# Performance work log

Hardware: AMD Instinct MI355X
Metric: run time of the kernel (lower is better)

Reference implementation:

```python
import jax, jax.numpy as jnp
import numpy as np

K = 32        # neighbors kept
SCALE = 1     # dilation stride for dilated kNN


def setup_inputs() -> dict:
    key = jax.random.key(0)
    ks = jax.random.split(key, 8)
    s = 0.05  # weight init scale
    return {
        "x": jax.random.normal(ks[0], (16, 3, 4096), jnp.float32),
        "w1": jax.random.normal(ks[1], (64, 3), jnp.float32) * s,
        "b1": jnp.zeros((64,), jnp.float32),
        "w2": jax.random.normal(ks[2], (128, 64), jnp.float32) * s,
        "b2": jnp.zeros((128,), jnp.float32),
        "w3": jax.random.normal(ks[3], (1024, 128), jnp.float32) * s,
        "b3": jnp.zeros((1024,), jnp.float32),
        "fw1": jax.random.normal(ks[4], (512, 1024), jnp.float32) * s,
        "fb1": jnp.zeros((512,), jnp.float32),
        "fw2": jax.random.normal(ks[5], (256, 512), jnp.float32) * s,
        "fb2": jnp.zeros((256,), jnp.float32),
        "fw3": jax.random.normal(ks[6], (9, 256), jnp.float32) * s,
        "fb3": jnp.zeros((9,), jnp.float32),
    }


def _knn_idx(x):
    # x: (B, C, N). Returns (B, N, K) indices of K nearest neighbors (dilated by SCALE).
    inner = jnp.einsum('bcn,bcm->bnm', x, x)            # (B, N, N)
    sq = jnp.sum(x * x, axis=1)                          # (B, N)
    neg_dist = 2.0 * inner - sq[:, :, None] - sq[:, None, :]  # = -||xi-xj||^2
    _, idx = jax.lax.top_k(neg_dist, K * SCALE)          # (B, N, K*SCALE)
    return idx[:, :, ::SCALE]                            # (B, N, K)


def reference(x, w1, b1, w2, b2, w3, b3, fw1, fb1, fw2, fb2, fw3, fb3):
    B, C, N = x.shape
    idx = _knn_idx(x)                                    # (B, N, K)
    xt = jnp.swapaxes(x, 1, 2)                           # (B, N, C)
    # gather neighbors: nbrs[b,n,k,c] = xt[b, idx[b,n,k], c]
    nbrs = jax.vmap(lambda xb, ib: xb[ib])(xt, idx)      # (B, N, K, C)
    x0 = nbrs - xt[:, :, None, :]                        # edge features x_j - x_i

    # STN (T-Net): shared MLP over edges, global max pool, FC head -> 3x3 transform
    h = jax.nn.relu(jnp.einsum('bnkc,oc->bnko', x0, w1) + b1)
    h = jax.nn.relu(jnp.einsum('bnkc,oc->bnko', h, w2) + b2)
    h = jax.nn.relu(jnp.einsum('bnkc,oc->bnko', h, w3) + b3)
    g = jnp.max(h, axis=(1, 2))                          # (B, 1024)
    f = jax.nn.relu(g @ fw1.T + fb1)
    f = jax.nn.relu(f @ fw2.T + fb2)
    t = (f @ fw3.T + fb3).reshape(B, 3, 3) + jnp.eye(3, dtype=x.dtype)

    out = jnp.einsum('bnc,bcd->bnd', xt, t)              # bmm(x^T, t)
    return jnp.swapaxes(out, 1, 2)                       # (B, 3, N)
```

## Files before the change

### kernel.cpp

```cpp
#include <hip/hip_runtime.h>
#include <hip/hip_fp8.h>

typedef __bf16 bf16_t;
typedef __bf16 bf16x8 __attribute__((ext_vector_type(8)));
typedef float floatx16 __attribute__((ext_vector_type(16)));
typedef int intx8 __attribute__((ext_vector_type(8)));
typedef unsigned long long u64;

#define B_ 16
#define N_ 4096
#define K_ 32


__device__ __forceinline__ unsigned enc_f(float f) {
    unsigned u = __float_as_uint(f);
    return (u & 0x80000000u) ? ~u : (u | 0x80000000u);
}
__device__ __forceinline__ float dec_f(unsigned e) {
    return __uint_as_float((e & 0x80000000u) ? (e & 0x7fffffffu) : ~e);
}

__device__ __forceinline__ float max3f(float a, float b, float c) {
    float d;
    asm("v_max3_f32 %0, %1, %2, %3" : "=v"(d) : "v"(a), "v"(b), "v"(c));
    return d;
}

__device__ __forceinline__ void ce(unsigned& a, unsigned& b) {
    const unsigned mn = a < b ? a : b;
    const unsigned mx = a < b ? b : a;
    a = mn; b = mx;
}

__global__ __launch_bounds__(512, 4) void knn_kernel(
    const float* __restrict__ x, const float* __restrict__ w3,
    const float* __restrict__ w2, unsigned short* __restrict__ idxb,
    unsigned* __restrict__ g_enc, unsigned char* __restrict__ w3f8,
    bf16_t* __restrict__ w2sw)
{
    __shared__ __align__(16) float4 cand[16 * 257];
    unsigned* lists = (unsigned*)cand;
    unsigned* m1 = ((unsigned*)cand) + 8192;
    const int tid = threadIdx.x;
    const int bid = blockIdx.x;

    {
        const int g = bid * 512 + tid;
        if (g < 131072) {
            const int j  = g & 31;
            const int lI = (g >> 5) & 63;
            const int kq = (g >> 11) & 1;
            const int cb = g >> 12;
            const int mt2 = kq * 2 + (j >> 4), q = j & 15;
            const int lmI = lI & 31, hiI = lI >> 5;
            const int ch = mt2 * 32 + (q & 3) + 8 * (q >> 2) + 4 * hiI;
            __hip_fp8_e4m3 t(16.0f * w3[(cb * 32 + lmI) * 128 + ch]);
            w3f8[g] = t.__x;
        } else if (g < 139264) {
            const int o = g - 131072;
            const int f = o >> 9, r = o & 511, lI = r >> 3, jj = r & 7;
            const int ks = f & 3, nb = f >> 2, lmI = lI & 31, hiI = lI >> 5;
            const int ic = ks * 16 + 4 * hiI + 8 * (jj >> 2) + (jj & 3);
            w2sw[o] = (bf16_t)w2[(nb * 32 + lmI) * 64 + ic];
        } else if (g < 155648) {
            g_enc[g - 139264] = 0u;
        }
    }

    const int b  = bid >> 7;
    const int q  = tid >> 4;
    const int n  = (bid & 127) * 32 + q;
    const int t  = tid & 15;
    const float* xb = x + b * 3 * N_;

    for (int j = tid; j < N_; j += 512) {
        float cx = xb[j], cy = xb[N_ + j], cz = xb[2 * N_ + j];
        cand[j + (j >> 8)] = make_float4(-2.f * cx, -2.f * cy, -2.f * cz,
                                         fmaf(cx, cx, fmaf(cy, cy, cz * cz)));
    }
    __syncthreads();

    const float xi0 = xb[n], xi1 = xb[N_ + n], xi2 = xb[2 * N_ + n];
    const float xisq1 = fmaf(xi0, xi0, fmaf(xi1, xi1, xi2 * xi2)) + 1.0f;

    unsigned r[8];
    #pragma unroll
    for (int s = 0; s < 8; s++) r[s] = 0x7F7FFFFFu;

    const int j0 = t * 256;
    const int pb = t * 257;
    #pragma unroll 1
    for (int jb = 0; jb < 256; jb += 8) {
        unsigned k[8];
        #pragma unroll
        for (int u = 0; u < 8; u++) {
            const float4 c = cand[pb + jb + u];
            const float d = fmaf(c.z, xi2, fmaf(c.y, xi1, fmaf(c.x, xi0, c.w)));
            k[u] = (__float_as_uint(d + xisq1) & 0xFFFFF000u)
                 | (unsigned)(j0 + jb + u);
        }
        ce(k[0], k[1]); ce(k[2], k[3]); ce(k[4], k[5]); ce(k[6], k[7]);
        ce(k[0], k[2]); ce(k[1], k[3]); ce(k[4], k[6]); ce(k[5], k[7]);
        ce(k[1], k[2]); ce(k[5], k[6]);
        ce(k[0], k[4]); ce(k[1], k[5]); ce(k[2], k[6]); ce(k[3], k[7]);
        ce(k[2], k[4]); ce(k[3], k[5]);
        ce(k[1], k[2]); ce(k[3], k[4]); ce(k[5], k[6]);
        unsigned s[8];
        #pragma unroll
        for (int u = 0; u < 8; u++)
            s[u] = r[u] < k[7 - u] ? r[u] : k[7 - u];
        ce(s[0], s[4]); ce(s[1], s[5]); ce(s[2], s[6]); ce(s[3], s[7]);
        ce(s[0], s[2]); ce(s[1], s[3]); ce(s[4], s[6]); ce(s[5], s[7]);
        ce(s[0], s[1]); ce(s[2], s[3]); ce(s[4], s[5]); ce(s[6], s[7]);
        #pragma unroll
        for (int u = 0; u < 8; u++) r[u] = s[u];
    }
    __syncthreads();

    #pragma unroll
    for (int k = 0; k < 8; k++) lists[tid * 9 + k] = r[k];
    __syncthreads();

    if (tid < 128) {
        const int q1 = tid >> 2, gi = tid & 3;
        const int base = (q1 * 16 + gi * 4) * 9;
        unsigned h0 = lists[base], h1 = lists[base + 9];
        unsigned h2 = lists[base + 18], h3 = lists[base + 27];
        int p0 = 0, p1 = 0, p2 = 0, p3 = 0;
        unsigned* outp = m1 + (q1 * 4 + gi) * 32;
        #pragma unroll 1
        for (int k = 0; k < 32; k++) {
            const unsigned m01 = h0 < h1 ? h0 : h1;
            const unsigned m23 = h2 < h3 ? h2 : h3;
            const unsigned v = m01 < m23 ? m01 : m23;
            outp[k] = v;
            if (m01 < m23) {
                if (h1 < h0) { p1++; h1 = p1 < 8 ? lists[base + 9 + p1] : 0xFFFFFFFFu; }
                else         { p0++; h0 = p0 < 8 ? lists[base + p0]     : 0xFFFFFFFFu; }
            } else {
                if (h3 < h2) { p3++; h3 = p3 < 8 ? lists[base + 27 + p3] : 0xFFFFFFFFu; }
                else         { p2++; h2 = p2 < 8 ? lists[base + 18 + p2] : 0xFFFFFFFFu; }
            }
        }
    }
    __syncthreads();

    if (tid < 32) {
        const unsigned* g0 = m1 + tid * 128;
        unsigned h0 = g0[0], h1 = g0[32], h2 = g0[64], h3 = g0[96];
        int p0 = 0, p1 = 0, p2 = 0, p3 = 0;
        const int nq = (bid & 127) * 32 + tid;
        unsigned short* op = idxb + ((size_t)(b * N_ + nq)) * K_;
        #pragma unroll 1
        for (int k = 0; k < K_; k++) {
            const unsigned m01 = h0 < h1 ? h0 : h1;
            const unsigned m23 = h2 < h3 ? h2 : h3;
            const unsigned v = m01 < m23 ? m01 : m23;
            op[k] = (unsigned short)(v & 0xFFFu);
            if (m01 < m23) {
                if (h1 < h0) { p1++; h1 = p1 < 32 ? g0[32 + p1] : 0xFFFFFFFFu; }
                else         { p0++; h0 = p0 < 32 ? g0[p0]      : 0xFFFFFFFFu; }
            } else {
                if (h3 < h2) { p3++; h3 = p3 < 32 ? g0[96 + p3] : 0xFFFFFFFFu; }
                else         { p2++; h2 = p2 < 32 ? g0[64 + p2] : 0xFFFFFFFFu; }
            }
        }
    }
}

__device__ __forceinline__ void chunk_epilogue(
    const floatx16& a0, const floatx16& a1, int cb, unsigned* gl, int lm)
{
    float c0 = fmaxf(a0[0], a1[0]);
    float c1 = fmaxf(a0[1], a1[1]);
    float c2 = fmaxf(a0[2], a1[2]);
    float c3 = fmaxf(a0[3], a1[3]);
    #pragma unroll
    for (int o = 4; o < 16; o += 4) {
        c0 = max3f(a0[o + 0], a1[o + 0], c0);
        c1 = max3f(a0[o + 1], a1[o + 1], c1);
        c2 = max3f(a0[o + 2], a1[o + 2], c2);
        c3 = max3f(a0[o + 3], a1[o + 3], c3);
    }
    const float m = max3f(c0, c1, fmaxf(c2, c3));
    atomicMax(&gl[cb * 32 + lm], enc_f(m));
}

__global__ __launch_bounds__(256, 3) void mlp_kernel(
    const float* __restrict__ x, const unsigned short* __restrict__ idxb,
    const float* __restrict__ w1, const float* __restrict__ b1,
    const float* __restrict__ b2,
    const bf16_t* __restrict__ w2sw, const unsigned char* __restrict__ w3f8,
    unsigned* __restrict__ g_enc)
{
    __shared__ unsigned gl[1024];
    __shared__ __align__(16) float4 w1l[64];
    __shared__ __align__(16) float b2s[128];

    const int tid = threadIdx.x;
    const int b   = blockIdx.x >> 9;
    const int p0  = (blockIdx.x & 511) * 8;
    const float* xb = x + b * 3 * N_;

    const int wv = tid >> 6;
    const int l  = tid & 63;
    const int lm = l & 31;
    const int hi = l >> 5;

    for (int i = tid; i < 1024; i += 256) gl[i] = 0u;
    if (tid < 64)
        w1l[tid] = make_float4(w1[tid * 3], w1[tid * 3 + 1], w1[tid * 3 + 2], b1[tid]);
    else if (tid < 192)
        b2s[tid - 64] = 256.0f * b2[tid - 64];
    __syncthreads();

    const floatx16 zf = (floatx16)0.f;

    const unsigned char* w3p = w3f8 + l * 32;
#define PREFETCH_W3(dst, c) do {                                              \
        dst[0] = *(const intx8*)(w3p + (c) * 4096);                           \
        dst[1] = *(const intx8*)(w3p + (c) * 4096 + 2048);                    \
    } while (0)

    intx8 bwA[2], bwB[2];
    PREFETCH_W3(bwA, 0);

    float d0[2], d1[2], d2[2];
    #pragma unroll
    for (int nt2 = 0; nt2 < 2; nt2++) {
        const int pp = p0 + wv * 2 + nt2;
        const int j  = idxb[((size_t)(b * N_ + pp)) * K_ + lm];
        d0[nt2] = xb[j]          - xb[pp];
        d1[nt2] = xb[N_ + j]     - xb[N_ + pp];
        d2[nt2] = xb[2 * N_ + j] - xb[2 * N_ + pp];
    }

    bf16x8 a1f[2];
    #pragma unroll
    for (int tt = 0; tt < 2; tt++) {
        const float4 w = w1l[tt * 32 + lm];
        bf16x8 v = (bf16x8)(bf16_t)0.f;
        if (hi == 0) {
            v[0] = (bf16_t)w.x; v[1] = (bf16_t)w.y;
            v[2] = (bf16_t)w.z; v[3] = (bf16_t)w.w;
        }
        a1f[tt] = v;
    }

    bf16x8 b1h[2][4];
    #pragma unroll
    for (int nt2 = 0; nt2 < 2; nt2++) {
        bf16x8 bf = (bf16x8)(bf16_t)0.f;
        if (hi == 0) {
            bf[0] = (bf16_t)d0[nt2]; bf[1] = (bf16_t)d1[nt2];
            bf[2] = (bf16_t)d2[nt2]; bf[3] = (bf16_t)1.0f;
        }
        floatx16 hacc[2];
        hacc[0] = __builtin_amdgcn_mfma_f32_32x32x16_bf16(a1f[0], bf, zf, 0, 0, 0);
        hacc[1] = __builtin_amdgcn_mfma_f32_32x32x16_bf16(a1f[1], bf, zf, 0, 0, 0);
        #pragma unroll
        for (int ks = 0; ks < 4; ks++)
            #pragma unroll
            for (int jj = 0; jj < 8; jj++)
                b1h[nt2][ks][jj] = (bf16_t)fmaxf(
                    hacc[ks >> 1][(jj & 3) + 4 * (jj >> 2) + 8 * (ks & 1)], 0.f);
    }

    intx8 a3v[2][2];
    #pragma unroll
    for (int mt2 = 0; mt2 < 4; mt2++) {
        floatx16 acc0 = (floatx16)0.f, acc1 = (floatx16)0.f;
        #pragma unroll
        for (int ks = 0; ks < 4; ks++) {
            const bf16x8 aw = *(const bf16x8*)&w2sw[((mt2 * 4 + ks) * 64 + l) * 8];
            acc0 = __builtin_amdgcn_mfma_f32_32x32x16_bf16(aw, b1h[0][ks], acc0, 0, 0, 0);
            acc1 = __builtin_amdgcn_mfma_f32_32x32x16_bf16(aw, b1h[1][ks], acc1, 0, 0, 0);
        }
        const int kq = mt2 >> 1, c0 = (mt2 & 1) * 4;
        #pragma unroll
        for (int i2 = 0; i2 < 4; i2++) {
            const float4 bb = *(const float4*)&b2s[mt2 * 32 + i2 * 8 + hi * 4];
            {
                const float v0 = fmaxf(fmaf(acc0[4 * i2 + 0], 256.f, bb.x), 0.f);
                const float v1 = fmaxf(fmaf(acc0[4 * i2 + 1], 256.f, bb.y), 0.f);
                const float v2 = fmaxf(fmaf(acc0[4 * i2 + 2], 256.f, bb.z), 0.f);
                const float v3 = fmaxf(fmaf(acc0[4 * i2 + 3], 256.f, bb.w), 0.f);
                int w = __builtin_amdgcn_cvt_pk_fp8_f32(v0, v1, 0, false);
                w = __builtin_amdgcn_cvt_pk_fp8_f32(v2, v3, w, true);
                a3v[0][kq][c0 + i2] = w;
            }
            {
                const float v0 = fmaxf(fmaf(acc1[4 * i2 + 0], 256.f, bb.x), 0.f);
                const float v1 = fmaxf(fmaf(acc1[4 * i2 + 1], 256.f, bb.y), 0.f);
                const float v2 = fmaxf(fmaf(acc1[4 * i2 + 2], 256.f, bb.z), 0.f);
                const float v3 = fmaxf(fmaf(acc1[4 * i2 + 3], 256.f, bb.w), 0.f);
                int w = __builtin_amdgcn_cvt_pk_fp8_f32(v0, v1, 0, false);
                w = __builtin_amdgcn_cvt_pk_fp8_f32(v2, v3, w, true);
                a3v[1][kq][c0 + i2] = w;
            }
        }
    }

#define COMPUTE_W3(d0_, d1_, buf) do {                                        \
        __builtin_amdgcn_s_setprio(1);                                        \
        d0_ = __builtin_amdgcn_mfma_scale_f32_32x32x64_f8f6f4(                \
            a3v[0][0], buf[0], zf, 0, 0, 0, 0x7F7F7F7F, 0, 0x7F7F7F7F);       \
        d1_ = __builtin_amdgcn_mfma_scale_f32_32x32x64_f8f6f4(                \
            a3v[1][0], buf[0], zf, 0, 0, 0, 0x7F7F7F7F, 0, 0x7F7F7F7F);       \
        d0_ = __builtin_amdgcn_mfma_scale_f32_32x32x64_f8f6f4(                \
            a3v[0][1], buf[1], d0_, 0, 0, 0, 0x7F7F7F7F, 0, 0x7F7F7F7F);      \
        d1_ = __builtin_amdgcn_mfma_scale_f32_32x32x64_f8f6f4(                \
            a3v[1][1], buf[1], d1_, 0, 0, 0, 0x7F7F7F7F, 0, 0x7F7F7F7F);      \
        __builtin_amdgcn_s_setprio(0); } while (0)

    floatx16 pA0, pA1, pB0, pB1;

    PREFETCH_W3(bwB, 1);
    COMPUTE_W3(pA0, pA1, bwA);

    #pragma unroll 1
    for (int cc = 0; cc < 15; cc++) {
        PREFETCH_W3(bwA, 2 * cc + 2);
        COMPUTE_W3(pB0, pB1, bwB);
        chunk_epilogue(pA0, pA1, 2 * cc, gl, lm);
        PREFETCH_W3(bwB, 2 * cc + 3);
        COMPUTE_W3(pA0, pA1, bwA);
        chunk_epilogue(pB0, pB1, 2 * cc + 1, gl, lm);
    }
    COMPUTE_W3(pB0, pB1, bwB);
    chunk_epilogue(pA0, pA1, 30, gl, lm);
    chunk_epilogue(pB0, pB1, 31, gl, lm);

#undef PREFETCH_W3
#undef COMPUTE_W3

    __syncthreads();
    for (int i = tid; i < 1024; i += 256)
        atomicMax(&g_enc[b * 1024 + i], gl[i]);
}

__global__ __launch_bounds__(256) void head1_kernel(
    const unsigned* __restrict__ g_enc, const float* __restrict__ b3,
    const float* __restrict__ fw1, const float* __restrict__ fb1,
    float* __restrict__ f1buf)
{
    __shared__ __align__(16) float g[1024];
    __shared__ float red[256];
    const int t = threadIdx.x;
    const int b = blockIdx.x >> 3;
    const int s = blockIdx.x & 7;

    for (int i = t; i < 1024; i += 256)
        g[i] = fmaxf(fmaf(dec_f(g_enc[b * 1024 + i]), 2.44140625e-4f, b3[i]), 0.f);
    __syncthreads();

    const int o = s * 64 + (t & 63);
    const int quarter = t >> 6;
    const float4* wr = (const float4*)(fw1 + (size_t)o * 1024) + quarter * 64;
    const float4* gv = (const float4*)g + quarter * 64;
    float acc = 0.f;
    #pragma unroll 4
    for (int i = 0; i < 64; i++) {
        float4 a = wr[i], c = gv[i];
        acc = fmaf(a.x, c.x, acc); acc = fmaf(a.y, c.y, acc);
        acc = fmaf(a.z, c.z, acc); acc = fmaf(a.w, c.w, acc);
    }
    red[t] = acc;
    __syncthreads();
    if (t < 64) {
        const float v = red[t] + red[t + 64] + red[t + 128] + red[t + 192];
        f1buf[b * 512 + s * 64 + t] = fmaxf(v + fb1[s * 64 + t], 0.f);
    }
}

__global__ __launch_bounds__(256) void head2_kernel(
    const float* __restrict__ f1buf,
    const float* __restrict__ fw2, const float* __restrict__ fb2,
    const float* __restrict__ fw3, const float* __restrict__ fb3,
    float* __restrict__ tmat)
{
    __shared__ __align__(16) float f1[512];
    __shared__ __align__(16) float f2[256];
    const int t = threadIdx.x, b = blockIdx.x;

    if (t < 128) ((float4*)f1)[t] = ((const float4*)(f1buf + b * 512))[t];
    __syncthreads();
    {
        const int o = t;
        const float4* wr = (const float4*)(fw2 + (size_t)o * 512);
        const float4* fv = (const float4*)f1;
        float acc = fb2[o];
        for (int i = 0; i < 128; i++) {
            float4 a = wr[i], c = fv[i];
            acc = fmaf(a.x, c.x, acc); acc = fmaf(a.y, c.y, acc);
            acc = fmaf(a.z, c.z, acc); acc = fmaf(a.w, c.w, acc);
        }
        f2[o] = fmaxf(acc, 0.f);
    }
    __syncthreads();
    if (t < 9) {
        const float4* wr = (const float4*)(fw3 + (size_t)t * 256);
        const float4* fv = (const float4*)f2;
        float acc = fb3[t];
        for (int i = 0; i < 64; i++) {
            float4 a = wr[i], c = fv[i];
            acc = fmaf(a.x, c.x, acc); acc = fmaf(a.y, c.y, acc);
            acc = fmaf(a.z, c.z, acc); acc = fmaf(a.w, c.w, acc);
        }
        if (t == 0 || t == 4 || t == 8) acc += 1.f;
        tmat[b * 9 + t] = acc;
    }
}

__global__ __launch_bounds__(256) void out_kernel(
    const float* __restrict__ x, const float* __restrict__ tmat,
    float* __restrict__ out)
{
    const int gid = blockIdx.x * 256 + threadIdx.x;
    const int b = gid >> 12, n = gid & 4095;
    const float* T = tmat + b * 9;
    const float x0 = x[b * 12288 + n];
    const float x1 = x[b * 12288 + 4096 + n];
    const float x2 = x[b * 12288 + 8192 + n];
    #pragma unroll
    for (int d = 0; d < 3; d++)
        out[b * 12288 + d * 4096 + n] =
            fmaf(x2, T[6 + d], fmaf(x1, T[3 + d], x0 * T[d]));
}

extern "C" void kernel_launch(void* const* d_in, const int* in_sizes, int n_in,
                              void* d_out, int out_size, void* d_ws, size_t ws_size,
                              hipStream_t stream) {
    const float* x   = (const float*)d_in[0];
    const float* w1  = (const float*)d_in[1];
    const float* b1  = (const float*)d_in[2];
    const float* w2  = (const float*)d_in[3];
    const float* b2  = (const float*)d_in[4];
    const float* w3  = (const float*)d_in[5];
    const float* b3  = (const float*)d_in[6];
    const float* fw1 = (const float*)d_in[7];
    const float* fb1 = (const float*)d_in[8];
    const float* fw2 = (const float*)d_in[9];
    const float* fb2 = (const float*)d_in[10];
    const float* fw3 = (const float*)d_in[11];
    const float* fb3 = (const float*)d_in[12];
    float* out = (float*)d_out;

    char* ws = (char*)d_ws;
    unsigned short* idxb = (unsigned short*)ws;
    unsigned* g_enc = (unsigned*)(ws + 4194304);
    unsigned char* w3f8 = (unsigned char*)(ws + 4259840);
    bf16_t* w2sw = (bf16_t*)(ws + 4390912);
    float* tmat  = (float*)(ws + 4407296);
    float* f1buf = (float*)(ws + 4407872);

    knn_kernel<<<2048, 512, 0, stream>>>(x, w3, w2, idxb, g_enc, w3f8, w2sw);
    mlp_kernel<<<8192, 256, 0, stream>>>(x, idxb, w1, b1, b2, w2sw, w3f8, g_enc);
    head1_kernel<<<128, 256, 0, stream>>>(g_enc, b3, fw1, fb1, f1buf);
    head2_kernel<<<16, 256, 0, stream>>>(f1buf, fw2, fb2, fw3, fb3, tmat);
    out_kernel<<<256, 256, 0, stream>>>(x, tmat, out);
}
```

Measured before the change: 465.4 us.

## Process two queries per thread in kNN scan and reorder W3 prefetch pipeline

```diff
diff --git a/kernel.cpp b/kernel.cpp
--- a/kernel.cpp
+++ b/kernel.cpp
@@ -30,6 +30,26 @@
     const unsigned mn = a < b ? a : b;
     const unsigned mx = a < b ? b : a;
     a = mn; b = mx;
+}
+
+__device__ __forceinline__ void sort8(unsigned* k) {
+    ce(k[0], k[1]); ce(k[2], k[3]); ce(k[4], k[5]); ce(k[6], k[7]);
+    ce(k[0], k[2]); ce(k[1], k[3]); ce(k[4], k[6]); ce(k[5], k[7]);
+    ce(k[1], k[2]); ce(k[5], k[6]);
+    ce(k[0], k[4]); ce(k[1], k[5]); ce(k[2], k[6]); ce(k[3], k[7]);
+    ce(k[2], k[4]); ce(k[3], k[5]);
+    ce(k[1], k[2]); ce(k[3], k[4]); ce(k[5], k[6]);
+}
+__device__ __forceinline__ void merge_top8(unsigned* r, const unsigned* k) {
+    unsigned s[8];
+    #pragma unroll
+    for (int u = 0; u < 8; u++)
+        s[u] = r[u] < k[7 - u] ? r[u] : k[7 - u];
+    ce(s[0], s[4]); ce(s[1], s[5]); ce(s[2], s[6]); ce(s[3], s[7]);
+    ce(s[0], s[2]); ce(s[1], s[3]); ce(s[4], s[6]); ce(s[5], s[7]);
+    ce(s[0], s[1]); ce(s[2], s[3]); ce(s[4], s[5]); ce(s[6], s[7]);
+    #pragma unroll
+    for (int u = 0; u < 8; u++) r[u] = s[u];
 }
 
 __global__ __launch_bounds__(512, 4) void knn_kernel(
@@ -68,9 +88,8 @@
     }
 
     const int b  = bid >> 7;
-    const int q  = tid >> 4;
-    const int n  = (bid & 127) * 32 + q;
-    const int t  = tid & 15;
+    const int qp = tid >> 5;
+    const int ch = tid & 31;
     const float* xb = x + b * 3 * N_;
 
     for (int j = tid; j < N_; j += 512) {
@@ -80,54 +99,49 @@
     }
     __syncthreads();
 
-    const float xi0 = xb[n], xi1 = xb[N_ + n], xi2 = xb[2 * N_ + n];
-    const float xisq1 = fmaf(xi0, xi0, fmaf(xi1, xi1, xi2 * xi2)) + 1.0f;
-
-    unsigned r[8];
-    #pragma unroll
-    for (int s = 0; s < 8; s++) r[s] = 0x7F7FFFFFu;
-
-    const int j0 = t * 256;
-    const int pb = t * 257;
+    const int na = (bid & 127) * 32 + qp;
+    const int nb = na + 16;
+    const float qa0 = xb[na], qa1 = xb[N_ + na], qa2 = xb[2 * N_ + na];
+    const float qb0 = xb[nb], qb1 = xb[N_ + nb], qb2 = xb[2 * N_ + nb];
+    const float sqa = fmaf(qa0, qa0, fmaf(qa1, qa1, qa2 * qa2)) + 1.0f;
+    const float sqb = fmaf(qb0, qb0, fmaf(qb1, qb1, qb2 * qb2)) + 1.0f;
+
+    unsigned ra[8], rb[8];
+    #pragma unroll
+    for (int s = 0; s < 8; s++) { ra[s] = 0x7F7FFFFFu; rb[s] = 0x7F7FFFFFu; }
+
+    const int j0 = ch * 128;
+    const int pb = ch * 128 + (ch >> 1);
     #pragma unroll 1
-    for (int jb = 0; jb < 256; jb += 8) {
-        unsigned k[8];
+    for (int jb = 0; jb < 128; jb += 8) {
+        unsigned ka[8], kb[8];
         #pragma unroll
         for (int u = 0; u < 8; u++) {
             const float4 c = cand[pb + jb + u];
-            const float d = fmaf(c.z, xi2, fmaf(c.y, xi1, fmaf(c.x, xi0, c.w)));
-            k[u] = (__float_as_uint(d + xisq1) & 0xFFFFF000u)
-                 | (unsigned)(j0 + jb + u);
-        }
-        ce(k[0], k[1]); ce(k[2], k[3]); ce(k[4], k[5]); ce(k[6], k[7]);
-        ce(k[0], k[2]); ce(k[1], k[3]); ce(k[4], k[6]); ce(k[5], k[7]);
-        ce(k[1], k[2]); ce(k[5], k[6]);
-        ce(k[0], k[4]); ce(k[1], k[5]); ce(k[2], k[6]); ce(k[3], k[7]);
-        ce(k[2], k[4]); ce(k[3], k[5]);
-        ce(k[1], k[2]); ce(k[3], k[4]); ce(k[5], k[6]);
-        unsigned s[8];
-        #pragma unroll
-        for (int u = 0; u < 8; u++)
-            s[u] = r[u] < k[7 - u] ? r[u] : k[7 - u];
-        ce(s[0], s[4]); ce(s[1], s[5]); ce(s[2], s[6]); ce(s[3], s[7]);
-        ce(s[0], s[2]); ce(s[1], s[3]); ce(s[4], s[6]); ce(s[5], s[7]);
-        ce(s[0], s[1]); ce(s[2], s[3]); ce(s[4], s[5]); ce(s[6], s[7]);
-        #pragma unroll
-        for (int u = 0; u < 8; u++) r[u] = s[u];
-    }
-    __syncthreads();
-
-    #pragma unroll
-    for (int k = 0; k < 8; k++) lists[tid * 9 + k] = r[k];
-    __syncthreads();
-
-    if (tid < 128) {
-        const int q1 = tid >> 2, gi = tid & 3;
-        const int base = (q1 * 16 + gi * 4) * 9;
-        unsigned h0 = lists[base], h1 = lists[base + 9];
-        unsigned h2 = lists[base + 18], h3 = lists[base + 27];
+            const float da = fmaf(c.z, qa2, fmaf(c.y, qa1, fmaf(c.x, qa0, c.w)));
+            const float db = fmaf(c.z, qb2, fmaf(c.y, qb1, fmaf(c.x, qb0, c.w)));
+            ka[u] = (__float_as_uint(da + sqa) & 0xFFFFF000u) | (unsigned)(j0 + jb + u);
+            kb[u] = (__float_as_uint(db + sqb) & 0xFFFFF000u) | (unsigned)(j0 + jb + u);
+        }
+        sort8(ka); merge_top8(ra, ka);
+        sort8(kb); merge_top8(rb, kb);
+    }
+    __syncthreads();
+
+    #pragma unroll
+    for (int k = 0; k < 8; k++) {
+        lists[((qp * 32 + ch) << 3) + k]        = ra[k];
+        lists[(((qp + 16) * 32 + ch) << 3) + k] = rb[k];
+    }
+    __syncthreads();
+
+    if (tid < 256) {
+        const int q1 = tid >> 3, gi = tid & 7;
+        const int base = (q1 * 32 + gi * 4) * 8;
+        unsigned h0 = lists[base], h1 = lists[base + 8];
+        unsigned h2 = lists[base + 16], h3 = lists[base + 24];
         int p0 = 0, p1 = 0, p2 = 0, p3 = 0;
-        unsigned* outp = m1 + (q1 * 4 + gi) * 32;
+        unsigned* outp = m1 + (q1 * 8 + gi) * 32;
         #pragma unroll 1
         for (int k = 0; k < 32; k++) {
             const unsigned m01 = h0 < h1 ? h0 : h1;
@@ -135,28 +149,28 @@
             const unsigned v = m01 < m23 ? m01 : m23;
             outp[k] = v;
             if (m01 < m23) {
-                if (h1 < h0) { p1++; h1 = p1 < 8 ? lists[base + 9 + p1] : 0xFFFFFFFFu; }
-                else         { p0++; h0 = p0 < 8 ? lists[base + p0]     : 0xFFFFFFFFu; }
+                if (h1 < h0) { p1++; h1 = p1 < 8 ? lists[base + 8 + p1]  : 0xFFFFFFFFu; }
+                else         { p0++; h0 = p0 < 8 ? lists[base + p0]      : 0xFFFFFFFFu; }
             } else {
-                if (h3 < h2) { p3++; h3 = p3 < 8 ? lists[base + 27 + p3] : 0xFFFFFFFFu; }
-                else         { p2++; h2 = p2 < 8 ? lists[base + 18 + p2] : 0xFFFFFFFFu; }
+                if (h3 < h2) { p3++; h3 = p3 < 8 ? lists[base + 24 + p3] : 0xFFFFFFFFu; }
+                else         { p2++; h2 = p2 < 8 ? lists[base + 16 + p2] : 0xFFFFFFFFu; }
             }
         }
     }
     __syncthreads();
 
-    if (tid < 32) {
-        const unsigned* g0 = m1 + tid * 128;
+    if (tid < 64) {
+        const int q = tid >> 1, h = tid & 1;
+        const unsigned* g0 = m1 + (q * 8 + h * 4) * 32;
         unsigned h0 = g0[0], h1 = g0[32], h2 = g0[64], h3 = g0[96];
         int p0 = 0, p1 = 0, p2 = 0, p3 = 0;
-        const int nq = (bid & 127) * 32 + tid;
-        unsigned short* op = idxb + ((size_t)(b * N_ + nq)) * K_;
+        unsigned* outp = lists + (q * 2 + h) * 32;
         #pragma unroll 1
-        for (int k = 0; k < K_; k++) {
+        for (int k = 0; k < 32; k++) {
             const unsigned m01 = h0 < h1 ? h0 : h1;
             const unsigned m23 = h2 < h3 ? h2 : h3;
             const unsigned v = m01 < m23 ? m01 : m23;
-            op[k] = (unsigned short)(v & 0xFFFu);
+            outp[k] = v;
             if (m01 < m23) {
                 if (h1 < h0) { p1++; h1 = p1 < 32 ? g0[32 + p1] : 0xFFFFFFFFu; }
                 else         { p0++; h0 = p0 < 32 ? g0[p0]      : 0xFFFFFFFFu; }
@@ -164,6 +178,23 @@
                 if (h3 < h2) { p3++; h3 = p3 < 32 ? g0[96 + p3] : 0xFFFFFFFFu; }
                 else         { p2++; h2 = p2 < 32 ? g0[64 + p2] : 0xFFFFFFFFu; }
             }
+        }
+    }
+    __syncthreads();
+
+    if (tid < 32) {
+        const unsigned* A  = lists + (tid * 2) * 32;
+        const unsigned* Bl = lists + (tid * 2 + 1) * 32;
+        unsigned h0 = A[0], h1 = Bl[0];
+        int p0 = 0, p1 = 0;
+        const int nq = (bid & 127) * 32 + tid;
+        unsigned short* op = idxb + ((size_t)(b * N_ + nq)) * K_;
+        #pragma unroll 1
+        for (int k = 0; k < K_; k++) {
+            const unsigned v = h0 < h1 ? h0 : h1;
+            op[k] = (unsigned short)(v & 0xFFFu);
+            if (h1 < h0) { p1++; h1 = p1 < 32 ? Bl[p1] : 0xFFFFFFFFu; }
+            else         { p0++; h0 = p0 < 32 ? A[p0]  : 0xFFFFFFFFu; }
         }
     }
 }
@@ -317,16 +348,22 @@
 
     PREFETCH_W3(bwB, 1);
     COMPUTE_W3(pA0, pA1, bwA);
+    PREFETCH_W3(bwA, 2);
 
     #pragma unroll 1
-    for (int cc = 0; cc < 15; cc++) {
-        PREFETCH_W3(bwA, 2 * cc + 2);
+    for (int cc = 0; cc < 14; cc++) {
         COMPUTE_W3(pB0, pB1, bwB);
+        PREFETCH_W3(bwB, 2 * cc + 3);
         chunk_epilogue(pA0, pA1, 2 * cc, gl, lm);
-        PREFETCH_W3(bwB, 2 * cc + 3);
         COMPUTE_W3(pA0, pA1, bwA);
+        PREFETCH_W3(bwA, 2 * cc + 4);
         chunk_epilogue(pB0, pB1, 2 * cc + 1, gl, lm);
     }
+    COMPUTE_W3(pB0, pB1, bwB);
+    PREFETCH_W3(bwB, 31);
+    chunk_epilogue(pA0, pA1, 28, gl, lm);
+    COMPUTE_W3(pA0, pA1, bwA);
+    chunk_epilogue(pB0, pB1, 29, gl, lm);
     COMPUTE_W3(pB0, pB1, bwB);
     chunk_epilogue(pA0, pA1, 30, gl, lm);
     chunk_epilogue(pB0, pB1, 31, gl, lm);
```

Result: slower. 501.5 us (+7.7%).

## Fuse kNN selection with edge MLP and move weight prep to separate kernel

Applied to the files above, without the earlier changes.

```diff
diff --git a/kernel.cpp b/kernel.cpp
--- a/kernel.cpp
+++ b/kernel.cpp
@@ -32,45 +32,91 @@
     a = mn; b = mx;
 }
 
-__global__ __launch_bounds__(512, 4) void knn_kernel(
-    const float* __restrict__ x, const float* __restrict__ w3,
-    const float* __restrict__ w2, unsigned short* __restrict__ idxb,
+__device__ __forceinline__ void sort8(unsigned* k) {
+    ce(k[0], k[1]); ce(k[2], k[3]); ce(k[4], k[5]); ce(k[6], k[7]);
+    ce(k[0], k[2]); ce(k[1], k[3]); ce(k[4], k[6]); ce(k[5], k[7]);
+    ce(k[1], k[2]); ce(k[5], k[6]);
+    ce(k[0], k[4]); ce(k[1], k[5]); ce(k[2], k[6]); ce(k[3], k[7]);
+    ce(k[2], k[4]); ce(k[3], k[5]);
+    ce(k[1], k[2]); ce(k[3], k[4]); ce(k[5], k[6]);
+}
+__device__ __forceinline__ void merge_top8(unsigned* r, const unsigned* k) {
+    unsigned s[8];
+    #pragma unroll
+    for (int u = 0; u < 8; u++)
+        s[u] = r[u] < k[7 - u] ? r[u] : k[7 - u];
+    ce(s[0], s[4]); ce(s[1], s[5]); ce(s[2], s[6]); ce(s[3], s[7]);
+    ce(s[0], s[2]); ce(s[1], s[3]); ce(s[4], s[6]); ce(s[5], s[7]);
+    ce(s[0], s[1]); ce(s[2], s[3]); ce(s[4], s[5]); ce(s[6], s[7]);
+    #pragma unroll
+    for (int u = 0; u < 8; u++) r[u] = s[u];
+}
+
+__global__ __launch_bounds__(512) void prep_kernel(
+    const float* __restrict__ w3, const float* __restrict__ w2,
     unsigned* __restrict__ g_enc, unsigned char* __restrict__ w3f8,
     bf16_t* __restrict__ w2sw)
 {
-    __shared__ __align__(16) float4 cand[16 * 257];
-    unsigned* lists = (unsigned*)cand;
-    unsigned* m1 = ((unsigned*)cand) + 8192;
+    const int g = blockIdx.x * 512 + threadIdx.x;
+    if (g < 131072) {
+        const int j  = g & 31;
+        const int lI = (g >> 5) & 63;
+        const int kq = (g >> 11) & 1;
+        const int cb = g >> 12;
+        const int mt2 = kq * 2 + (j >> 4), q = j & 15;
+        const int lmI = lI & 31, hiI = lI >> 5;
+        const int ch = mt2 * 32 + (q & 3) + 8 * (q >> 2) + 4 * hiI;
+        __hip_fp8_e4m3 t(16.0f * w3[(cb * 32 + lmI) * 128 + ch]);
+        w3f8[g] = t.__x;
+    } else if (g < 139264) {
+        const int o = g - 131072;
+        const int f = o >> 9, r = o & 511, lI = r >> 3, jj = r & 7;
+        const int ks = f & 3, nb = f >> 2, lmI = lI & 31, hiI = lI >> 5;
+        const int ic = ks * 16 + 4 * hiI + 8 * (jj >> 2) + (jj & 3);
+        w2sw[o] = (bf16_t)w2[(nb * 32 + lmI) * 64 + ic];
+    } else if (g < 155648) {
+        g_enc[g - 139264] = 0u;
+    }
+}
+
+__device__ __forceinline__ void chunk_epilogue(
+    const floatx16& a0, const floatx16& a1, int cb, unsigned* gl, int lm)
+{
+    float c0 = fmaxf(a0[0], a1[0]);
+    float c1 = fmaxf(a0[1], a1[1]);
+    float c2 = fmaxf(a0[2], a1[2]);
+    float c3 = fmaxf(a0[3], a1[3]);
+    #pragma unroll
+    for (int o = 4; o < 16; o += 4) {
+        c0 = max3f(a0[o + 0], a1[o + 0], c0);
+        c1 = max3f(a0[o + 1], a1[o + 1], c1);
+        c2 = max3f(a0[o + 2], a1[o + 2], c2);
+        c3 = max3f(a0[o + 3], a1[o + 3], c3);
+    }
+    const float m = max3f(c0, c1, fmaxf(c2, c3));
+    atomicMax(&gl[cb * 32 + lm], enc_f(m));
+}
+
+__global__ __launch_bounds__(512, 4) void fused_kernel(
+    const float* __restrict__ x,
+    const float* __restrict__ w1, const float* __restrict__ b1,
+    const float* __restrict__ b2,
+    const bf16_t* __restrict__ w2sw, const unsigned char* __restrict__ w3f8,
+    unsigned* __restrict__ g_enc)
+{
+    __shared__ __align__(16) char smem[65792];
+    float4* cand = (float4*)smem;
+    unsigned* lists = (unsigned*)smem;
+    unsigned* m1 = ((unsigned*)smem) + 8192;
+    unsigned short* idxl = (unsigned short*)smem;
+    unsigned* gl = (unsigned*)(smem + 2048);
+    float4* w1l = (float4*)(smem + 6144);
+    float* b2s = (float*)(smem + 7168);
+
     const int tid = threadIdx.x;
     const int bid = blockIdx.x;
-
-    {
-        const int g = bid * 512 + tid;
-        if (g < 131072) {
-            const int j  = g & 31;
-            const int lI = (g >> 5) & 63;
-            const int kq = (g >> 11) & 1;
-            const int cb = g >> 12;
-            const int mt2 = kq * 2 + (j >> 4), q = j & 15;
-            const int lmI = lI & 31, hiI = lI >> 5;
-            const int ch = mt2 * 32 + (q & 3) + 8 * (q >> 2) + 4 * hiI;
-            __hip_fp8_e4m3 t(16.0f * w3[(cb * 32 + lmI) * 128 + ch]);
-            w3f8[g] = t.__x;
-        } else if (g < 139264) {
-            const int o = g - 131072;
-            const int f = o >> 9, r = o & 511, lI = r >> 3, jj = r & 7;
-            const int ks = f & 3, nb = f >> 2, lmI = lI & 31, hiI = lI >> 5;
-            const int ic = ks * 16 + 4 * hiI + 8 * (jj >> 2) + (jj & 3);
-            w2sw[o] = (bf16_t)w2[(nb * 32 + lmI) * 64 + ic];
-        } else if (g < 155648) {
-            g_enc[g - 139264] = 0u;
-        }
-    }
-
-    const int b  = bid >> 7;
-    const int q  = tid >> 4;
-    const int n  = (bid & 127) * 32 + q;
-    const int t  = tid & 15;
+    const int b = bid >> 7;
+    const int pbase = (bid & 127) * 32;
     const float* xb = x + b * 3 * N_;
 
     for (int j = tid; j < N_; j += 512) {
@@ -80,45 +126,37 @@
     }
     __syncthreads();
 
-    const float xi0 = xb[n], xi1 = xb[N_ + n], xi2 = xb[2 * N_ + n];
-    const float xisq1 = fmaf(xi0, xi0, fmaf(xi1, xi1, xi2 * xi2)) + 1.0f;
-
-    unsigned r[8];
-    #pragma unroll
-    for (int s = 0; s < 8; s++) r[s] = 0x7F7FFFFFu;
-
-    const int j0 = t * 256;
-    const int pb = t * 257;
-    #pragma unroll 1
-    for (int jb = 0; jb < 256; jb += 8) {
-        unsigned k[8];
-        #pragma unroll
-        for (int u = 0; u < 8; u++) {
-            const float4 c = cand[pb + jb + u];
-            const float d = fmaf(c.z, xi2, fmaf(c.y, xi1, fmaf(c.x, xi0, c.w)));
-            k[u] = (__float_as_uint(d + xisq1) & 0xFFFFF000u)
-                 | (unsigned)(j0 + jb + u);
-        }
-        ce(k[0], k[1]); ce(k[2], k[3]); ce(k[4], k[5]); ce(k[6], k[7]);
-        ce(k[0], k[2]); ce(k[1], k[3]); ce(k[4], k[6]); ce(k[5], k[7]);
-        ce(k[1], k[2]); ce(k[5], k[6]);
-        ce(k[0], k[4]); ce(k[1], k[5]); ce(k[2], k[6]); ce(k[3], k[7]);
-        ce(k[2], k[4]); ce(k[3], k[5]);
-        ce(k[1], k[2]); ce(k[3], k[4]); ce(k[5], k[6]);
-        unsigned s[8];
-        #pragma unroll
-        for (int u = 0; u < 8; u++)
-            s[u] = r[u] < k[7 - u] ? r[u] : k[7 - u];
-        ce(s[0], s[4]); ce(s[1], s[5]); ce(s[2], s[6]); ce(s[3], s[7]);
-        ce(s[0], s[2]); ce(s[1], s[3]); ce(s[4], s[6]); ce(s[5], s[7]);
-        ce(s[0], s[1]); ce(s[2], s[3]); ce(s[4], s[5]); ce(s[6], s[7]);
-        #pragma unroll
-        for (int u = 0; u < 8; u++) r[u] = s[u];
-    }
-    __syncthreads();
-
-    #pragma unroll
-    for (int k = 0; k < 8; k++) lists[tid * 9 + k] = r[k];
+    {
+        const int q = tid >> 4;
+        const int n = pbase + q;
+        const int t = tid & 15;
+        const float xi0 = xb[n], xi1 = xb[N_ + n], xi2 = xb[2 * N_ + n];
+        const float xisq1 = fmaf(xi0, xi0, fmaf(xi1, xi1, xi2 * xi2)) + 1.0f;
+
+        unsigned r[8];
+        #pragma unroll
+        for (int s = 0; s < 8; s++) r[s] = 0x7F7FFFFFu;
+
+        const int j0 = t * 256;
+        const int pb = t * 257;
+        #pragma unroll 1
+        for (int jb = 0; jb < 256; jb += 8) {
+            unsigned k[8];
+            #pragma unroll
+            for (int u = 0; u < 8; u++) {
+                const float4 c = cand[pb + jb + u];
+                const float d = fmaf(c.z, xi2, fmaf(c.y, xi1, fmaf(c.x, xi0, c.w)));
+                k[u] = (__float_as_uint(d + xisq1) & 0xFFFFF000u)
+                     | (unsigned)(j0 + jb + u);
+            }
+            sort8(k);
+            merge_top8(r, k);
+        }
+        __syncthreads();
+
+        #pragma unroll
+        for (int k = 0; k < 8; k++) lists[tid * 9 + k] = r[k];
+    }
     __syncthreads();
 
     if (tid < 128) {
@@ -149,8 +187,7 @@
         const unsigned* g0 = m1 + tid * 128;
         unsigned h0 = g0[0], h1 = g0[32], h2 = g0[64], h3 = g0[96];
         int p0 = 0, p1 = 0, p2 = 0, p3 = 0;
-        const int nq = (bid & 127) * 32 + tid;
-        unsigned short* op = idxb + ((size_t)(b * N_ + nq)) * K_;
+        unsigned short* op = idxl + tid * 32;
         #pragma unroll 1
         for (int k = 0; k < K_; k++) {
             const unsigned m01 = h0 < h1 ? h0 : h1;
@@ -165,141 +202,27 @@
                 else         { p2++; h2 = p2 < 32 ? g0[64 + p2] : 0xFFFFFFFFu; }
             }
         }
-    }
-}
-
-__device__ __forceinline__ void chunk_epilogue(
-    const floatx16& a0, const floatx16& a1, int cb, unsigned* gl, int lm)
-{
-    float c0 = fmaxf(a0[0], a1[0]);
-    float c1 = fmaxf(a0[1], a1[1]);
-    float c2 = fmaxf(a0[2], a1[2]);
-    float c3 = fmaxf(a0[3], a1[3]);
-    #pragma unroll
-    for (int o = 4; o < 16; o += 4) {
-        c0 = max3f(a0[o + 0], a1[o + 0], c0);
-        c1 = max3f(a0[o + 1], a1[o + 1], c1);
-        c2 = max3f(a0[o + 2], a1[o + 2], c2);
-        c3 = max3f(a0[o + 3], a1[o + 3], c3);
-    }
-    const float m = max3f(c0, c1, fmaxf(c2, c3));
-    atomicMax(&gl[cb * 32 + lm], enc_f(m));
-}
-
-__global__ __launch_bounds__(256, 3) void mlp_kernel(
-    const float* __restrict__ x, const unsigned short* __restrict__ idxb,
-    const float* __restrict__ w1, const float* __restrict__ b1,
-    const float* __restrict__ b2,
-    const bf16_t* __restrict__ w2sw, const unsigned char* __restrict__ w3f8,
-    unsigned* __restrict__ g_enc)
-{
-    __shared__ unsigned gl[1024];
-    __shared__ __align__(16) float4 w1l[64];
-    __shared__ __align__(16) float b2s[128];
-
-    const int tid = threadIdx.x;
-    const int b   = blockIdx.x >> 9;
-    const int p0  = (blockIdx.x & 511) * 8;
-    const float* xb = x + b * 3 * N_;
+    } else if (tid >= 64 && tid < 128) {
+        const int i = tid - 64;
+        w1l[i] = make_float4(w1[i * 3], w1[i * 3 + 1], w1[i * 3 + 2], b1[i]);
+    } else if (tid >= 128 && tid < 256) {
+        b2s[tid - 128] = 256.0f * b2[tid - 128];
+    } else if (tid >= 256) {
+        for (int ii = tid - 256; ii < 1024; ii += 256) gl[ii] = 0u;
+    }
+    __syncthreads();
 
     const int wv = tid >> 6;
     const int l  = tid & 63;
     const int lm = l & 31;
     const int hi = l >> 5;
-
-    for (int i = tid; i < 1024; i += 256) gl[i] = 0u;
-    if (tid < 64)
-        w1l[tid] = make_float4(w1[tid * 3], w1[tid * 3 + 1], w1[tid * 3 + 2], b1[tid]);
-    else if (tid < 192)
-        b2s[tid - 64] = 256.0f * b2[tid - 64];
-    __syncthreads();
-
     const floatx16 zf = (floatx16)0.f;
-
     const unsigned char* w3p = w3f8 + l * 32;
+
 #define PREFETCH_W3(dst, c) do {                                              \
         dst[0] = *(const intx8*)(w3p + (c) * 4096);                           \
         dst[1] = *(const intx8*)(w3p + (c) * 4096 + 2048);                    \
     } while (0)
-
-    intx8 bwA[2], bwB[2];
-    PREFETCH_W3(bwA, 0);
-
-    float d0[2], d1[2], d2[2];
-    #pragma unroll
-    for (int nt2 = 0; nt2 < 2; nt2++) {
-        const int pp = p0 + wv * 2 + nt2;
-        const int j  = idxb[((size_t)(b * N_ + pp)) * K_ + lm];
-        d0[nt2] = xb[j]          - xb[pp];
-        d1[nt2] = xb[N_ + j]     - xb[N_ + pp];
-        d2[nt2] = xb[2 * N_ + j] - xb[2 * N_ + pp];
-    }
-
-    bf16x8 a1f[2];
-    #pragma unroll
-    for (int tt = 0; tt < 2; tt++) {
-        const float4 w = w1l[tt * 32 + lm];
-        bf16x8 v = (bf16x8)(bf16_t)0.f;
-        if (hi == 0) {
-            v[0] = (bf16_t)w.x; v[1] = (bf16_t)w.y;
-            v[2] = (bf16_t)w.z; v[3] = (bf16_t)w.w;
-        }
-        a1f[tt] = v;
-    }
-
-    bf16x8 b1h[2][4];
-    #pragma unroll
-    for (int nt2 = 0; nt2 < 2; nt2++) {
-        bf16x8 bf = (bf16x8)(bf16_t)0.f;
-        if (hi == 0) {
-            bf[0] = (bf16_t)d0[nt2]; bf[1] = (bf16_t)d1[nt2];
-            bf[2] = (bf16_t)d2[nt2]; bf[3] = (bf16_t)1.0f;
-        }
-        floatx16 hacc[2];
-        hacc[0] = __builtin_amdgcn_mfma_f32_32x32x16_bf16(a1f[0], bf, zf, 0, 0, 0);
-        hacc[1] = __builtin_amdgcn_mfma_f32_32x32x16_bf16(a1f[1], bf, zf, 0, 0, 0);
-        #pragma unroll
-        for (int ks = 0; ks < 4; ks++)
-            #pragma unroll
-            for (int jj = 0; jj < 8; jj++)
-                b1h[nt2][ks][jj] = (bf16_t)fmaxf(
-                    hacc[ks >> 1][(jj & 3) + 4 * (jj >> 2) + 8 * (ks & 1)], 0.f);
-    }
-
-    intx8 a3v[2][2];
-    #pragma unroll
-    for (int mt2 = 0; mt2 < 4; mt2++) {
-        floatx16 acc0 = (floatx16)0.f, acc1 = (floatx16)0.f;
-        #pragma unroll
-        for (int ks = 0; ks < 4; ks++) {
-            const bf16x8 aw = *(const bf16x8*)&w2sw[((mt2 * 4 + ks) * 64 + l) * 8];
-            acc0 = __builtin_amdgcn_mfma_f32_32x32x16_bf16(aw, b1h[0][ks], acc0, 0, 0, 0);
-            acc1 = __builtin_amdgcn_mfma_f32_32x32x16_bf16(aw, b1h[1][ks], acc1, 0, 0, 0);
-        }
-        const int kq = mt2 >> 1, c0 = (mt2 & 1) * 4;
-        #pragma unroll
-        for (int i2 = 0; i2 < 4; i2++) {
-            const float4 bb = *(const float4*)&b2s[mt2 * 32 + i2 * 8 + hi * 4];
-            {
-                const float v0 = fmaxf(fmaf(acc0[4 * i2 + 0], 256.f, bb.x), 0.f);
-                const float v1 = fmaxf(fmaf(acc0[4 * i2 + 1], 256.f, bb.y), 0.f);
-                const float v2 = fmaxf(fmaf(acc0[4 * i2 + 2], 256.f, bb.z), 0.f);
-                const float v3 = fmaxf(fmaf(acc0[4 * i2 + 3], 256.f, bb.w), 0.f);
-                int w = __builtin_amdgcn_cvt_pk_fp8_f32(v0, v1, 0, false);
-                w = __builtin_amdgcn_cvt_pk_fp8_f32(v2, v3, w, true);
-                a3v[0][kq][c0 + i2] = w;
-            }
-            {
-                const float v0 = fmaxf(fmaf(acc1[4 * i2 + 0], 256.f, bb.x), 0.f);
-                const float v1 = fmaxf(fmaf(acc1[4 * i2 + 1], 256.f, bb.y), 0.f);
-                const float v2 = fmaxf(fmaf(acc1[4 * i2 + 2], 256.f, bb.z), 0.f);
-                const float v3 = fmaxf(fmaf(acc1[4 * i2 + 3], 256.f, bb.w), 0.f);
-                int w = __builtin_amdgcn_cvt_pk_fp8_f32(v0, v1, 0, false);
-                w = __builtin_amdgcn_cvt_pk_fp8_f32(v2, v3, w, true);
-                a3v[1][kq][c0 + i2] = w;
-            }
-        }
-    }
 
 #define COMPUTE_W3(d0_, d1_, buf) do {                                        \
         __builtin_amdgcn_s_setprio(1);                                        \
@@ -313,29 +236,110 @@
             a3v[1][1], buf[1], d1_, 0, 0, 0, 0x7F7F7F7F, 0, 0x7F7F7F7F);      \
         __builtin_amdgcn_s_setprio(0); } while (0)
 
-    floatx16 pA0, pA1, pB0, pB1;
-
-    PREFETCH_W3(bwB, 1);
-    COMPUTE_W3(pA0, pA1, bwA);
-
     #pragma unroll 1
-    for (int cc = 0; cc < 15; cc++) {
-        PREFETCH_W3(bwA, 2 * cc + 2);
+    for (int it = 0; it < 2; it++) {
+        intx8 bwA[2], bwB[2];
+        PREFETCH_W3(bwA, 0);
+
+        float d0[2], d1[2], d2[2];
+        #pragma unroll
+        for (int nt2 = 0; nt2 < 2; nt2++) {
+            const int lp = wv * 4 + it * 2 + nt2;
+            const int pp = pbase + lp;
+            const int j  = idxl[lp * 32 + lm];
+            d0[nt2] = xb[j]          - xb[pp];
+            d1[nt2] = xb[N_ + j]     - xb[N_ + pp];
+            d2[nt2] = xb[2 * N_ + j] - xb[2 * N_ + pp];
+        }
+
+        bf16x8 a1f[2];
+        #pragma unroll
+        for (int tt = 0; tt < 2; tt++) {
+            const float4 w = w1l[tt * 32 + lm];
+            bf16x8 v = (bf16x8)(bf16_t)0.f;
+            if (hi == 0) {
+                v[0] = (bf16_t)w.x; v[1] = (bf16_t)w.y;
+                v[2] = (bf16_t)w.z; v[3] = (bf16_t)w.w;
+            }
+            a1f[tt] = v;
+        }
+
+        bf16x8 b1h[2][4];
+        #pragma unroll
+        for (int nt2 = 0; nt2 < 2; nt2++) {
+            bf16x8 bf = (bf16x8)(bf16_t)0.f;
+            if (hi == 0) {
+                bf[0] = (bf16_t)d0[nt2]; bf[1] = (bf16_t)d1[nt2];
+                bf[2] = (bf16_t)d2[nt2]; bf[3] = (bf16_t)1.0f;
+            }
+            floatx16 hacc[2];
+            hacc[0] = __builtin_amdgcn_mfma_f32_32x32x16_bf16(a1f[0], bf, zf, 0, 0, 0);
+            hacc[1] = __builtin_amdgcn_mfma_f32_32x32x16_bf16(a1f[1], bf, zf, 0, 0, 0);
+            #pragma unroll
+            for (int ks = 0; ks < 4; ks++)
+                #pragma unroll
+                for (int jj = 0; jj < 8; jj++)
+                    b1h[nt2][ks][jj] = (bf16_t)fmaxf(
+                        hacc[ks >> 1][(jj & 3) + 4 * (jj >> 2) + 8 * (ks & 1)], 0.f);
+        }
+
+        intx8 a3v[2][2];
+        #pragma unroll
+        for (int mt2 = 0; mt2 < 4; mt2++) {
+            floatx16 acc0 = (floatx16)0.f, acc1 = (floatx16)0.f;
+            #pragma unroll
+            for (int ks = 0; ks < 4; ks++) {
+                const bf16x8 aw = *(const bf16x8*)&w2sw[((mt2 * 4 + ks) * 64 + l) * 8];
+                acc0 = __builtin_amdgcn_mfma_f32_32x32x16_bf16(aw, b1h[0][ks], acc0, 0, 0, 0);
+                acc1 = __builtin_amdgcn_mfma_f32_32x32x16_bf16(aw, b1h[1][ks], acc1, 0, 0, 0);
+            }
+            const int kq = mt2 >> 1, c0 = (mt2 & 1) * 4;
+            #pragma unroll
+            for (int i2 = 0; i2 < 4; i2++) {
+                const float4 bb = *(const float4*)&b2s[mt2 * 32 + i2 * 8 + hi * 4];
+                {
+                    const float v0 = fmaxf(fmaf(acc0[4 * i2 + 0], 256.f, bb.x), 0.f);
+                    const float v1 = fmaxf(fmaf(acc0[4 * i2 + 1], 256.f, bb.y), 0.f);
+                    const float v2 = fmaxf(fmaf(acc0[4 * i2 + 2], 256.f, bb.z), 0.f);
+                    const float v3 = fmaxf(fmaf(acc0[4 * i2 + 3], 256.f, bb.w), 0.f);
+                    int w = __builtin_amdgcn_cvt_pk_fp8_f32(v0, v1, 0, false);
+                    w = __builtin_amdgcn_cvt_pk_fp8_f32(v2, v3, w, true);
+                    a3v[0][kq][c0 + i2] = w;
+                }
+                {
+                    const float v0 = fmaxf(fmaf(acc1[4 * i2 + 0], 256.f, bb.x), 0.f);
+                    const float v1 = fmaxf(fmaf(acc1[4 * i2 + 1], 256.f, bb.y), 0.f);
+                    const float v2 = fmaxf(fmaf(acc1[4 * i2 + 2], 256.f, bb.z), 0.f);
+                    const float v3 = fmaxf(fmaf(acc1[4 * i2 + 3], 256.f, bb.w), 0.f);
+                    int w = __builtin_amdgcn_cvt_pk_fp8_f32(v0, v1, 0, false);
+                    w = __builtin_amdgcn_cvt_pk_fp8_f32(v2, v3, w, true);
+                    a3v[1][kq][c0 + i2] = w;
+                }
+            }
+        }
+
+        floatx16 pA0, pA1, pB0, pB1;
+        PREFETCH_W3(bwB, 1);
+        COMPUTE_W3(pA0, pA1, bwA);
+        #pragma unroll 1
+        for (int cc = 0; cc < 15; cc++) {
+            PREFETCH_W3(bwA, 2 * cc + 2);
+            COMPUTE_W3(pB0, pB1, bwB);
+            chunk_epilogue(pA0, pA1, 2 * cc, gl, lm);
+            PREFETCH_W3(bwB, 2 * cc + 3);
+            COMPUTE_W3(pA0, pA1, bwA);
+            chunk_epilogue(pB0, pB1, 2 * cc + 1, gl, lm);
+        }
         COMPUTE_W3(pB0, pB1, bwB);
-        chunk_epilogue(pA0, pA1, 2 * cc, gl, lm);
-        PREFETCH_W3(bwB, 2 * cc + 3);
-        COMPUTE_W3(pA0, pA1, bwA);
-        chunk_epilogue(pB0, pB1, 2 * cc + 1, gl, lm);
-    }
-    COMPUTE_W3(pB0, pB1, bwB);
-    chunk_epilogue(pA0, pA1, 30, gl, lm);
-    chunk_epilogue(pB0, pB1, 31, gl, lm);
+        chunk_epilogue(pA0, pA1, 30, gl, lm);
+        chunk_epilogue(pB0, pB1, 31, gl, lm);
+    }
 
 #undef PREFETCH_W3
 #undef COMPUTE_W3
 
     __syncthreads();
-    for (int i = tid; i < 1024; i += 256)
+    for (int i = tid; i < 1024; i += 512)
         atomicMax(&g_enc[b * 1024 + i], gl[i]);
 }
 
@@ -447,15 +451,14 @@
     float* out = (float*)d_out;
 
     char* ws = (char*)d_ws;
-    unsigned short* idxb = (unsigned short*)ws;
     unsigned* g_enc = (unsigned*)(ws + 4194304);
     unsigned char* w3f8 = (unsigned char*)(ws + 4259840);
     bf16_t* w2sw = (bf16_t*)(ws + 4390912);
     float* tmat  = (float*)(ws + 4407296);
     float* f1buf = (float*)(ws + 4407872);
 
-    knn_kernel<<<2048, 512, 0, stream>>>(x, w3, w2, idxb, g_enc, w3f8, w2sw);
-    mlp_kernel<<<8192, 256, 0, stream>>>(x, idxb, w1, b1, b2, w2sw, w3f8, g_enc);
+    prep_kernel<<<304, 512, 0, stream>>>(w3, w2, g_enc, w3f8, w2sw);
+    fused_kernel<<<2048, 512, 0, stream>>>(x, w1, b1, b2, w2sw, w3f8, g_enc);
     head1_kernel<<<128, 256, 0, stream>>>(g_enc, b3, fw1, fb1, f1buf);
     head2_kernel<<<16, 256, 0, stream>>>(f1buf, fw2, fb2, fw3, fb3, tmat);
     out_kernel<<<256, 256, 0, stream>>>(x, tmat, out);
```

After: 1.017 ms. 119% more time.
